# Kernel optimization log

Hardware: AMD Instinct MI355X
Metric: run time of the kernel (lower is better)

Reference implementation:

```python
import jax, jax.numpy as jnp
import numpy as np

C = 32          # in_channels
K = 16          # cluster_nums
G = 16          # grid size per axis (64 / window 4)
FW = 4          # window size
H = G * FW      # 64
NG = G ** 3     # 4096 nodes
NC = NG // K    # 256 nodes per cluster (balanced)
EPS = 1e-5


def setup_inputs():
    key = jax.random.key(0)
    ks = jax.random.split(key, 10)
    def w(k, shape, s=0.05):
        return jax.random.normal(k, shape, jnp.float32) * s
    # balanced cluster assignment (each cluster has exactly NC nodes)
    rng = np.random.RandomState(0)
    ci = np.repeat(np.arange(K, dtype=np.int32), NC)
    rng.shuffle(ci)
    return {
        "x_concat": jax.random.normal(ks[0], (1, H, H, H, C), jnp.float32),
        "cluster_index": jnp.asarray(ci),
        # per-cluster Adjacent_matrix params (1x1 conv == per-pixel linear)
        "conv1_w": w(ks[1], (K, 2 * C, C)), "conv1_b": jnp.zeros((K, 2 * C)),
        "bn1_g": jnp.ones((K, 2 * C)), "bn1_b": jnp.zeros((K, 2 * C)),
        "conv2_w": w(ks[2], (K, 3 * C, 2 * C)), "conv2_b": jnp.zeros((K, 3 * C)),
        "bn2_g": jnp.ones((K, 3 * C)), "bn2_b": jnp.zeros((K, 3 * C)),
        "conv3_w": w(ks[3], (K, 3 * C)), "conv3_b": jnp.zeros((K,)),
        # per-cluster GCN params
        "gcn_w": w(ks[4], (K, 2 * C, C)),
        "bn3_g": jnp.ones((K, C)), "bn3_b": jnp.zeros((K, C)),
        # shared MLP producing spatial weight [C,C] from centroid
        "mlp_w1": w(ks[5], (C, C * C // 8)), "mlp_b1": jnp.zeros((C * C // 8,)),
        "mlp_w2": w(ks[6], (C * C // 8, C * C // 4)), "mlp_b2": jnp.zeros((C * C // 4,)),
        "mlp_w3": w(ks[7], (C * C // 4, C * C)), "mlp_b3": jnp.zeros((C * C,)),
    }


def _bn(h, g, b, axes):
    # train-mode BatchNorm (biased batch statistics), dropout treated as eval/no-op
    m = h.mean(axes, keepdims=True)
    v = h.var(axes, keepdims=True)
    return (h - m) * jax.lax.rsqrt(v + EPS) * g + b


def _forward(cluster_index, x_concat, conv1_w, conv1_b, bn1_g, bn1_b,
             conv2_w, conv2_b, bn2_g, bn2_b, conv3_w, conv3_b,
             gcn_w, bn3_g, bn3_b,
             mlp_w1, mlp_b1, mlp_w2, mlp_b2, mlp_w3, mlp_b3):
    # window_partition + mean over windows -> [NG, C] node features
    x = x_concat.reshape(1, G, FW, G, FW, G, FW, C).mean(axis=(2, 4, 6)).reshape(NG, C)
    order = jnp.argsort(cluster_index)  # stable: contiguous per-cluster index blocks
    eye = jnp.eye(NC, dtype=x.dtype)
    outs = []
    for i in range(K):  # fixed structural loop over clusters
        idx = order[i * NC:(i + 1) * NC]
        xi = x[idx]                                  # [n, C]
        cent = xi.mean(0)                            # kmeans centroid of cluster
        h = jax.nn.relu(cent @ mlp_w1 + mlp_b1)
        h = jax.nn.relu(h @ mlp_w2 + mlp_b2)
        sw = jax.nn.sigmoid(h @ mlp_w3 + mlp_b3).reshape(C, C)
        # Adjacent_matrix: pairwise |xi - xj| -> 1x1 conv stack -> softmax adjacency
        d = jnp.abs(xi[:, None, :] - xi[None, :, :])  # [n, n, C]
        a = jax.nn.leaky_relu(_bn(jnp.einsum('ijc,oc->ijo', d, conv1_w[i]) + conv1_b[i],
                                  bn1_g[i], bn1_b[i], (0, 1)), 0.2)
        a = jax.nn.leaky_relu(_bn(jnp.einsum('ijc,oc->ijo', a, conv2_w[i]) + conv2_b[i],
                                  bn2_g[i], bn2_b[i], (0, 1)), 0.2)
        logits = jnp.einsum('ijc,c->ij', a, conv3_w[i]) + conv3_b[i]  # symmetric
        adj = jax.nn.softmax(logits - 1e8 * eye, axis=-1)
        # gmul_GCN with edge ops [eye, adj] -> concat([x, adj @ x])
        agg = jnp.concatenate([xi, adj @ xi], axis=-1)  # [n, 2C]
        hi = jax.nn.leaky_relu(agg @ (gcn_w[i] @ sw), 0.2)
        hi = _bn(hi, bn3_g[i], bn3_b[i], (0,))          # BatchNorm1d over nodes
        outs.append(hi)
    # scatter_restore
    x_new = jnp.zeros((NG, C), x.dtype).at[order].set(jnp.concatenate(outs, 0))
    # back to grid, pad (1,2) per spatial dim, unfold 4-windows stride 1
    xg = x_new.reshape(1, G, G, G, C).transpose(0, 4, 1, 2, 3)  # [1,C,G,G,G]
    xp = jnp.pad(xg, ((0, 0), (0, 0), (1, 2), (1, 2), (1, 2)))
    iw = jnp.arange(G)[:, None] + jnp.arange(FW)[None, :]       # [G, FW]
    t = xp[:, :, iw]          # [1,C,G,FW,Gp,Gp]
    t = t[:, :, :, :, iw]     # [1,C,G,FW,G,FW,Gp]
    t = t[..., iw]            # [1,C,G,FW,G,FW,G,FW]
    out = t.transpose(0, 2, 3, 4, 5, 6, 7, 1).reshape(1, H, H, H, C)
    return out + x_concat


def reference(x_concat, cluster_index, conv1_w, conv1_b, bn1_g, bn1_b,
              conv2_w, conv2_b, bn2_g, bn2_b, conv3_w, conv3_b,
              gcn_w, bn3_g, bn3_b,
              mlp_w1, mlp_b1, mlp_w2, mlp_b2, mlp_w3, mlp_b3):
    return _forward(cluster_index, x_concat, conv1_w, conv1_b, bn1_g, bn1_b,
                    conv2_w, conv2_b, bn2_g, bn2_b, conv3_w, conv3_b,
                    gcn_w, bn3_g, bn3_b,
                    mlp_w1, mlp_b1, mlp_w2, mlp_b2, mlp_w3, mlp_b3)
```

## Files before the change

### kernel.cpp

```cpp
#include <hip/hip_runtime.h>
#include <hip/hip_bf16.h>


typedef short bfrag8 __attribute__((ext_vector_type(8)));
typedef float f32x4  __attribute__((ext_vector_type(4)));
typedef int   i32x4  __attribute__((ext_vector_type(4)));
typedef short s4v    __attribute__((ext_vector_type(4)));

#define DI __device__ __forceinline__

DI unsigned short f2bf(float f) {
  return __builtin_bit_cast(unsigned short, __float2bfloat16(f));
}
DI float bf2f(unsigned short u) {
  return __builtin_bit_cast(float, ((unsigned)u) << 16);
}
DI unsigned pack2bf(float lo, float hi) {
  unsigned ulo = __builtin_bit_cast(unsigned, lo) + 0x8000u;
  unsigned uhi = __builtin_bit_cast(unsigned, hi) + 0x8000u;
  return __builtin_amdgcn_perm(uhi, ulo, 0x07060302u);
}
DI bfrag8 scale_frag(bfrag8 v, float sc) {
  i32x4 wi = __builtin_bit_cast(i32x4, v);
  i32x4 o;
#pragma unroll
  for (int j = 0; j < 4; ++j) {
    unsigned u = (unsigned)wi[j];
    float lo = bf2f((unsigned short)(u & 0xffffu));
    float hi = bf2f((unsigned short)(u >> 16));
    o[j] = (int)pack2bf(lo * sc, hi * sc);
  }
  return __builtin_bit_cast(bfrag8, o);
}

__global__ __launch_bounds__(256) void k_prep(
    const float* __restrict__ xc, float* __restrict__ x,
    const float* __restrict__ w1, const float* __restrict__ w2,
    unsigned short* __restrict__ w1b, unsigned short* __restrict__ w2p,
    float* __restrict__ statsz) {
  const int bid = blockIdx.x, tid = threadIdx.x;
  if (bid < 128) {
    int idx = bid * 256 + tid;
    int c4 = idx & 7, g = idx >> 3;
    int gz = g & 15, gy = (g >> 4) & 15, gx = g >> 8;
    f32x4 s = {0.f, 0.f, 0.f, 0.f};
    for (int ix = 0; ix < 4; ++ix)
      for (int iy = 0; iy < 4; ++iy)
        for (int iz = 0; iz < 4; ++iz) {
          int X = gx * 4 + ix, Y = gy * 4 + iy, Z = gz * 4 + iz;
          s += *(const f32x4*)&xc[(size_t)(((X << 6) | Y) << 6 | Z) * 32 + c4 * 4];
        }
    *(f32x4*)&x[(size_t)idx * 4] = s * (1.f / 64.f);
    if (bid < 24) statsz[bid * 256 + tid] = 0.f;
  } else {
    int i = (bid - 128) * 256 + tid;
    if (i < 32768) w1b[i] = f2bf(w1[i]);
    int o = i >> 6, cc = i & 63;
    int s = cc >> 5, kp = cc & 31;
    int src = 32 * s + 16 * ((kp >> 2) & 1) + 4 * (kp >> 3) + (kp & 3);
    w2p[i] = f2bf(w2[(size_t)o * 64 + src]);
  }
}

__global__ __launch_bounds__(256) void k_order(
    const int* __restrict__ ci, const float* __restrict__ x,
    int* __restrict__ order, int* __restrict__ inv, float* __restrict__ xi,
    unsigned short* __restrict__ xib, float* __restrict__ centb) {
  const int k = blockIdx.x, t = threadIdx.x;
  __shared__ int scnt[256];
  __shared__ int ordl[256];
  __shared__ unsigned short xls[256 * 36];
  __shared__ float red[256];

  int match[16];
  int cnt = 0;
#pragma unroll
  for (int j = 0; j < 16; ++j) { match[j] = (ci[t * 16 + j] == k); cnt += match[j]; }
  scnt[t] = cnt;
  __syncthreads();
  for (int off = 1; off < 256; off <<= 1) {
    int v = (t >= off) ? scnt[t - off] : 0;
    __syncthreads();
    scnt[t] += v;
    __syncthreads();
  }
  int pos = scnt[t] - cnt;
#pragma unroll
  for (int j = 0; j < 16; ++j)
    if (match[j]) ordl[pos++] = t * 16 + j;
  __syncthreads();
  int src = ordl[t];
  order[k * 256 + t] = src;
  inv[src] = k * 256 + t;
  const f32x4* xr = (const f32x4*)(x + (size_t)src * 32);
  f32x4* xo = (f32x4*)(xi + ((size_t)k * 256 + t) * 32);
  uint2* xb = (uint2*)(xib + ((size_t)k * 256 + t) * 32);
  uint2* xl = (uint2*)&xls[t * 36];
#pragma unroll
  for (int c = 0; c < 8; ++c) {
    f32x4 v = xr[c];
    xo[c] = v;
    unsigned int lo = f2bf(v[0]) | ((unsigned)f2bf(v[1]) << 16);
    unsigned int hi = f2bf(v[2]) | ((unsigned)f2bf(v[3]) << 16);
    xb[c] = make_uint2(lo, hi);
    xl[c] = make_uint2(lo, hi);
  }
  __syncthreads();

  {
    int c = t & 31, rp = t >> 5;
    float ssum = 0.f;
    for (int r = rp; r < 256; r += 8) ssum += bf2f(xls[r * 36 + c]);
    red[t] = ssum;
  }
  __syncthreads();
  if (t < 32) {
    float tot = 0.f;
#pragma unroll
    for (int g = 0; g < 8; ++g) tot += red[g * 32 + t];
    centb[k * 32 + t] = tot * (1.f / 256.f);
  }
}

__global__ __launch_bounds__(256) void k_mlp(
    const float* __restrict__ centb,
    const float* __restrict__ mw1, const float* __restrict__ mb1,
    const float* __restrict__ mw2, const float* __restrict__ mb2,
    const float* __restrict__ mw3, const float* __restrict__ mb3,
    float* __restrict__ swb) {
  const int k = blockIdx.y, bx = blockIdx.x, t = threadIdx.x;
  __shared__ float cent[32];
  __shared__ float h1[128];
  __shared__ float h2s[256];
  __shared__ float red[256];
  if (t < 32) cent[t] = centb[k * 32 + t];
  __syncthreads();
  if (t < 128) {
    float s = mb1[t];
#pragma unroll
    for (int c = 0; c < 32; ++c) s += cent[c] * mw1[c * 128 + t];
    h1[t] = fmaxf(s, 0.f);
  }
  __syncthreads();
  {
    float s = mb2[t];
    for (int j = 0; j < 128; ++j) s += h1[j] * mw2[j * 256 + t];
    h2s[t] = fmaxf(s, 0.f);
  }
  __syncthreads();
  const int o = bx * 64 + (t & 63);
  const int part = t >> 6;
  float s = 0.f;
  const float* m3 = mw3 + (size_t)(part * 64) * 1024 + o;
#pragma unroll 8
  for (int j = 0; j < 64; ++j) s += h2s[part * 64 + j] * m3[j * 1024];
  red[t] = s;
  __syncthreads();
  if (t < 64) {
    float tot = red[t] + red[t + 64] + red[t + 128] + red[t + 192] + mb3[o];
    swb[k * 1024 + o] = 1.f / (1.f + __expf(-tot));
  }
}

template <int MODE>
__global__ __launch_bounds__(256, (MODE == 1) ? 3 : 4) void k_conv01(
    const float* __restrict__ xi,
    const unsigned short* __restrict__ w1b,
    const unsigned short* __restrict__ w2p,
    float* stats1, float* stats2,
    const float* __restrict__ bn1g, const float* __restrict__ bn1b) {
  const int k   = blockIdx.y;
  const int t36 = blockIdx.x;
  int a = 0, rem = t36;
  while (rem >= 8 - a) { rem -= 8 - a; ++a; }
  const int b = a + rem;
  const float w = (a == b) ? 1.f : 2.f;

  const int tid = threadIdx.x;
  const int lane = tid & 63;
  const int wv  = tid >> 6;
  const int l15 = lane & 15;
  const int lg  = lane >> 4;
  const int Pb0 = a * 32, Qb = b * 32;

  constexpr int NF  = (MODE == 0) ? 4 : 6;
  constexpr int NCH = NF * 4;

  __shared__ __align__(16) float xp[32][32];
  __shared__ float sred[192];
  __shared__ __align__(16) float s1s[(MODE == 1) ? 64 : 1];
  __shared__ __align__(16) float t1s[(MODE == 1) ? 64 : 1];

  const float* xik = xi + (size_t)k * 8192;
  {
    int r = tid >> 3, c4 = (tid & 7) * 4;
    *(f32x4*)&xp[r][c4] = *(const f32x4*)(xik + (size_t)(Pb0 + r) * 32 + c4);
  }
  if (tid < 192) sred[tid] = 0.f;
  if constexpr (MODE == 1) {
    if (tid >= 192) {
      const int ch = tid - 192;
      float sum = stats1[k * 128 + 2 * ch], sqv = stats1[k * 128 + 2 * ch + 1];
      float mean = sum * (1.f / 16384.f);
      float var  = sqv * (1.f / 16384.f) - mean * mean;
      float s = bn1g[k * 64 + ch] * rsqrtf(fmaxf(var, 0.f) + 1e-5f);
      s1s[ch] = s;
      t1s[ch] = bn1b[k * 64 + ch] - mean * s;
    }
  }

  float qv[2][8];
#pragma unroll
  for (int qg = 0; qg < 2; ++qg) {
    const f32x4* src = (const f32x4*)(xik + (size_t)(Qb + qg * 16 + l15) * 32 + lg * 8);
    f32x4 v0 = src[0], v1 = src[1];
#pragma unroll
    for (int j = 0; j < 4; ++j) { qv[qg][j] = v0[j]; qv[qg][4 + j] = v1[j]; }
  }

  bfrag8 B1[4];
  {
    const unsigned short* w1k = w1b + k * 2048;
#pragma unroll
    for (int f = 0; f < 4; ++f)
      B1[f] = *(const bfrag8*)(w1k + (16 * f + l15) * 32 + lg * 8);
  }
  bfrag8 B2[6][2];
  if constexpr (MODE == 1) {
    const unsigned short* w2k = w2p + k * 6144;
#pragma unroll
    for (int f2 = 0; f2 < 6; ++f2) {
      B2[f2][0] = *(const bfrag8*)(w2k + (16 * f2 + l15) * 64 + lg * 8);
      B2[f2][1] = *(const bfrag8*)(w2k + (16 * f2 + l15) * 64 + 32 + lg * 8);
    }
  }

  float ss[24], sq[24];
#pragma unroll
  for (int i = 0; i < 24; ++i) { ss[i] = 0.f; sq[i] = 0.f; }

  __syncthreads();

  if constexpr (MODE == 1) {
#pragma unroll
    for (int f = 0; f < 4; ++f)
      B1[f] = scale_frag(B1[f], s1s[16 * f + l15]);
  }

  const f32x4 z = {0.f, 0.f, 0.f, 0.f};

  bfrag8 dfa[4];
#pragma unroll
  for (int rp = 0; rp < 4; ++rp) {
    const int pl = rp >> 1, qg = rp & 1;
    const int plocal = wv * 8 + pl * 4;
    const float* xpp = &xp[plocal][lg * 8];
    f32x4 p0 = *(const f32x4*)xpp;
    f32x4 p1 = *(const f32x4*)(xpp + 4);
    float pvv[8];
#pragma unroll
    for (int j = 0; j < 4; ++j) { pvv[j] = p0[j]; pvv[4 + j] = p1[j]; }
    unsigned dw[4];
#pragma unroll
    for (int wj = 0; wj < 4; ++wj) {
      float d0 = fabsf(qv[qg][2 * wj]     - pvv[2 * wj]);
      float d1 = fabsf(qv[qg][2 * wj + 1] - pvv[2 * wj + 1]);
      dw[wj] = pack2bf(d0, d1);
    }
    i32x4 dwi = {(int)dw[0], (int)dw[1], (int)dw[2], (int)dw[3]};
    dfa[rp] = __builtin_bit_cast(bfrag8, dwi);
  }

#pragma unroll
  for (int rp = 0; rp < 4; ++rp) {
    f32x4 acc1[4];
    __builtin_amdgcn_s_setprio(1);
#pragma unroll
    for (int f = 0; f < 4; ++f) {
      f32x4 cin;
      if constexpr (MODE == 0) cin = z;
      else cin = *(const f32x4*)&t1s[16 * f + 4 * lg];
      acc1[f] = __builtin_amdgcn_mfma_f32_16x16x32_bf16(B1[f], dfa[rp], cin, 0, 0, 0);
    }
    __builtin_amdgcn_s_setprio(0);

    if constexpr (MODE == 0) {
#pragma unroll
      for (int f = 0; f < 4; ++f)
#pragma unroll
        for (int r = 0; r < 4; ++r) {
          float h = acc1[f][r];
          ss[f * 4 + r] += h; sq[f * 4 + r] = fmaf(h, h, sq[f * 4 + r]);
        }
    } else {
      unsigned paw[8];
#pragma unroll
      for (int f = 0; f < 4; ++f) {
        float h0 = acc1[f][0], h1 = acc1[f][1], h2 = acc1[f][2], h3 = acc1[f][3];
        h0 = fmaxf(h0, 0.2f * h0); h1 = fmaxf(h1, 0.2f * h1);
        h2 = fmaxf(h2, 0.2f * h2); h3 = fmaxf(h3, 0.2f * h3);
        paw[f * 2]     = pack2bf(h0, h1);
        paw[f * 2 + 1] = pack2bf(h2, h3);
      }
      i32x4 pa0i = {(int)paw[0], (int)paw[1], (int)paw[2], (int)paw[3]};
      i32x4 pa1i = {(int)paw[4], (int)paw[5], (int)paw[6], (int)paw[7]};
      bfrag8 pa0 = __builtin_bit_cast(bfrag8, pa0i);
      bfrag8 pa1 = __builtin_bit_cast(bfrag8, pa1i);

      __builtin_amdgcn_s_setprio(1);
#pragma unroll
      for (int f2 = 0; f2 < 6; ++f2) {
        f32x4 acc = __builtin_amdgcn_mfma_f32_16x16x32_bf16(B2[f2][0], pa0, z, 0, 0, 0);
        acc = __builtin_amdgcn_mfma_f32_16x16x32_bf16(B2[f2][1], pa1, acc, 0, 0, 0);
#pragma unroll
        for (int r = 0; r < 4; ++r) {
          float h = acc[r];
          ss[f2 * 4 + r] += h; sq[f2 * 4 + r] = fmaf(h, h, sq[f2 * 4 + r]);
        }
      }
      __builtin_amdgcn_s_setprio(0);
    }
  }

#pragma unroll
  for (int i = 0; i < NCH; ++i) {
#pragma unroll
    for (int m = 1; m <= 8; m <<= 1) {
      ss[i] += __shfl_xor(ss[i], m);
      sq[i] += __shfl_xor(sq[i], m);
    }
  }
  if (l15 == 0) {
#pragma unroll
    for (int i = 0; i < NCH; ++i) {
      int ch = 16 * (i >> 2) + 4 * lg + (i & 3);
      atomicAdd(&sred[ch * 2 + 0], ss[i] * w);
      atomicAdd(&sred[ch * 2 + 1], sq[i] * w);
    }
  }
  __syncthreads();
  float* gs = (MODE == 0) ? stats1 : stats2;
  if (tid < 2 * 16 * NF) atomicAdd(&gs[k * (2 * 16 * NF) + tid], sred[tid]);
}

__global__ __launch_bounds__(256, 4) void k_conv2(
    const float* __restrict__ xi,
    const unsigned short* __restrict__ w1b,
    const unsigned short* __restrict__ w2p,
    const float* __restrict__ stats1, const float* __restrict__ stats2,
    const float* __restrict__ bn1g, const float* __restrict__ bn1b,
    const float* __restrict__ bn2g, const float* __restrict__ bn2b,
    const float* __restrict__ c3w,
    float* __restrict__ logits) {
  const int k  = blockIdx.y;
  const int bx = blockIdx.x;
  const int tid = threadIdx.x;
  const int lane = tid & 63;
  const int wv  = tid >> 6;
  const int l15 = lane & 15;
  const int lg  = lane >> 4;

  __shared__ __align__(16) float xp[16][32];
  __shared__ __align__(16) float s1s[64];
  __shared__ __align__(16) float t1s[64];
  __shared__ __align__(16) float sw2s[96];
  __shared__ __align__(16) float cb2s[96];
  __shared__ __align__(16) float s42s[96];
  __shared__ float lt[16][17];

  const float* xik = xi + (size_t)k * 8192;

  if (tid < 64) {
    const int ch = tid;
    float sum = stats1[k * 128 + 2 * ch], sqv = stats1[k * 128 + 2 * ch + 1];
    float mean = sum * (1.f / 16384.f);
    float var  = sqv * (1.f / 16384.f) - mean * mean;
    float s = bn1g[k * 64 + ch] * rsqrtf(fmaxf(var, 0.f) + 1e-5f);
    s1s[ch] = s;
    t1s[ch] = bn1b[k * 64 + ch] - mean * s;
  } else if (tid < 160) {
    const int ch = tid - 64;
    float sum = stats2[k * 192 + 2 * ch], sqv = stats2[k * 192 + 2 * ch + 1];
    float mean = sum * (1.f / 16384.f);
    float var  = sqv * (1.f / 16384.f) - mean * mean;
    float s2 = bn2g[k * 96 + ch] * rsqrtf(fmaxf(var, 0.f) + 1e-5f);
    float t2 = bn2b[k * 96 + ch] - mean * s2;
    float w3 = c3w[k * 96 + ch];
    sw2s[ch] = s2 * w3;
    cb2s[ch] = t2 * w3;
    s42s[ch] = copysignf(0.4f, w3);
  }

  bfrag8 B1[4];
  {
    const unsigned short* w1k = w1b + k * 2048;
#pragma unroll
    for (int f = 0; f < 4; ++f)
      B1[f] = *(const bfrag8*)(w1k + (16 * f + l15) * 32 + lg * 8);
  }
  bfrag8 B2[6][2];
  {
    const unsigned short* w2k = w2p + k * 6144;
#pragma unroll
    for (int f2 = 0; f2 < 6; ++f2) {
      B2[f2][0] = *(const bfrag8*)(w2k + (16 * f2 + l15) * 64 + lg * 8);
      B2[f2][1] = *(const bfrag8*)(w2k + (16 * f2 + l15) * 64 + 32 + lg * 8);
    }
  }
  __syncthreads();
#pragma unroll
  for (int f = 0; f < 4; ++f)
    B1[f] = scale_frag(B1[f], s1s[16 * f + l15]);
#pragma unroll
  for (int f2 = 0; f2 < 6; ++f2) {
    float sc = sw2s[16 * f2 + l15];
    B2[f2][0] = scale_frag(B2[f2][0], sc);
    B2[f2][1] = scale_frag(B2[f2][1], sc);
  }

  for (int st = bx; st < 144; st += 64) {
    const int t36 = st >> 2, sub = st & 3;
    int a = 0, rem = t36;
    while (rem >= 8 - a) { rem -= 8 - a; ++a; }
    const int b = a + rem;
    const int Pb0 = a * 32 + (sub >> 1) * 16;
    const int Qb  = b * 32 + (sub & 1) * 16;

    __syncthreads();
    if (tid < 128) {
      int r = tid >> 3, c4 = (tid & 7) * 4;
      *(f32x4*)&xp[r][c4] = *(const f32x4*)(xik + (size_t)(Pb0 + r) * 32 + c4);
    }
    __syncthreads();

    float qv8[8];
    {
      const f32x4* src = (const f32x4*)(xik + (size_t)(Qb + l15) * 32 + lg * 8);
      f32x4 v0 = src[0], v1 = src[1];
#pragma unroll
      for (int j = 0; j < 4; ++j) { qv8[j] = v0[j]; qv8[4 + j] = v1[j]; }
    }

#pragma unroll
    for (int rp = 0; rp < 4; ++rp) {
      const int plocal = wv * 4 + rp;
      const int pglob  = Pb0 + plocal;

      const float* xpp = &xp[plocal][lg * 8];
      f32x4 p0 = *(const f32x4*)xpp;
      f32x4 p1 = *(const f32x4*)(xpp + 4);
      float pvv[8];
#pragma unroll
      for (int j = 0; j < 4; ++j) { pvv[j] = p0[j]; pvv[4 + j] = p1[j]; }
      unsigned dw[4];
#pragma unroll
      for (int wj = 0; wj < 4; ++wj) {
        float d0 = fabsf(qv8[2 * wj]     - pvv[2 * wj]);
        float d1 = fabsf(qv8[2 * wj + 1] - pvv[2 * wj + 1]);
        dw[wj] = pack2bf(d0, d1);
      }
      i32x4 dwi = {(int)dw[0], (int)dw[1], (int)dw[2], (int)dw[3]};
      bfrag8 df = __builtin_bit_cast(bfrag8, dwi);

      f32x4 acc1[4];
      __builtin_amdgcn_s_setprio(1);
#pragma unroll
      for (int f = 0; f < 4; ++f) {
        f32x4 cin = *(const f32x4*)&t1s[16 * f + 4 * lg];
        acc1[f] = __builtin_amdgcn_mfma_f32_16x16x32_bf16(B1[f], df, cin, 0, 0, 0);
      }
      __builtin_amdgcn_s_setprio(0);

      unsigned paw[8];
#pragma unroll
      for (int f = 0; f < 4; ++f) {
        float h0 = acc1[f][0], h1 = acc1[f][1], h2 = acc1[f][2], h3 = acc1[f][3];
        h0 = fmaxf(h0, 0.2f * h0); h1 = fmaxf(h1, 0.2f * h1);
        h2 = fmaxf(h2, 0.2f * h2); h3 = fmaxf(h3, 0.2f * h3);
        paw[f * 2]     = pack2bf(h0, h1);
        paw[f * 2 + 1] = pack2bf(h2, h3);
      }
      i32x4 pa0i = {(int)paw[0], (int)paw[1], (int)paw[2], (int)paw[3]};
      i32x4 pa1i = {(int)paw[4], (int)paw[5], (int)paw[6], (int)paw[7]};
      bfrag8 pa0 = __builtin_bit_cast(bfrag8, pa0i);
      bfrag8 pa1 = __builtin_bit_cast(bfrag8, pa1i);

      float lp = 0.f;
      __builtin_amdgcn_s_setprio(1);
#pragma unroll
      for (int f2 = 0; f2 < 6; ++f2) {
        f32x4 cin = *(const f32x4*)&cb2s[16 * f2 + 4 * lg];
        f32x4 acc = __builtin_amdgcn_mfma_f32_16x16x32_bf16(B2[f2][0], pa0, cin, 0, 0, 0);
        acc = __builtin_amdgcn_mfma_f32_16x16x32_bf16(B2[f2][1], pa1, acc, 0, 0, 0);
        f32x4 s4 = *(const f32x4*)&s42s[16 * f2 + 4 * lg];
#pragma unroll
        for (int r = 0; r < 4; ++r) {
          float aa = acc[r];
          float ab = fmaxf(aa, -aa);
          lp = fmaf(0.6f, aa, lp);
          lp = fmaf(s4[r], ab, lp);
        }
      }
      __builtin_amdgcn_s_setprio(0);
      lp += __shfl_xor(lp, 16);
      lp += __shfl_xor(lp, 32);
      if (lg == 0) {
        logits[(size_t)k * 65536 + (size_t)pglob * 256 + Qb + l15] = lp;
        lt[plocal][l15] = lp;
      }
    }

    __syncthreads();
    if (a != b) {
      const int ql = tid >> 4, pl = tid & 15;
      logits[(size_t)k * 65536 + (size_t)(Qb + ql) * 256 + Pb0 + pl] = lt[pl][ql];
    }
  }
}

__global__ __launch_bounds__(256) void k_graph(
    const unsigned short* __restrict__ xib,
    const float* __restrict__ logits,
    const float* __restrict__ swb,
    const float* __restrict__ gcnw,
    float* __restrict__ hi,
    float* __restrict__ stats3) {
  const int k  = blockIdx.y;
  const int pc = blockIdx.x;
  const int tid = threadIdx.x;
  __shared__ __align__(16) unsigned char smem[40960];
  unsigned short* xis = (unsigned short*)smem;
  float* wks  = (float*)(smem + 20480);
  float* cbuf = (float*)(smem + 28672);

  {
    const s4v* src = (const s4v*)(xib + (size_t)k * 8192 + tid * 32);
    s4v* dst = (s4v*)&xis[tid * 40];
#pragma unroll
    for (int j = 0; j < 8; ++j) dst[j] = src[j];
  }
  float* swl = cbuf;
  float* gks = cbuf + 1024;
#pragma unroll
  for (int j = 0; j < 4; ++j) swl[tid + j * 256] = swb[k * 1024 + tid + j * 256];
#pragma unroll
  for (int j = 0; j < 8; ++j) gks[tid + j * 256] = gcnw[(size_t)k * 2048 + tid + j * 256];
  __syncthreads();

#pragma unroll
  for (int j = 0; j < 8; ++j) {
    int e = tid + j * 256;
    int u = e >> 5, v = e & 31;
    float s = 0.f;
#pragma unroll
    for (int c = 0; c < 32; ++c) s += gks[u * 32 + c] * swl[c * 32 + v];
    wks[e] = s;
  }
  __syncthreads();

  float* es    = cbuf;
  float* axs   = cbuf + 2080;
  float* inv_s = cbuf + 2352;
  float* s3    = cbuf + 2360;
  if (tid < 64) s3[tid] = 0.f;

  const int row = tid >> 5;
  const int s   = tid & 31;
  const int pglob = pc * 8 + row;
  const float* lrow = logits + (size_t)k * 65536 + (size_t)pglob * 256;

  float m = -1e30f;
  for (int q = s; q < 256; q += 32) {
    float v = lrow[q];
    m = (q == pglob) ? m : fmaxf(m, v);
  }
#pragma unroll
  for (int mm = 1; mm < 32; mm <<= 1) m = fmaxf(m, __shfl_xor(m, mm));
  float sum = 0.f;
  for (int q = s; q < 256; q += 32) {
    float e = (q == pglob) ? 0.f : __expf(lrow[q] - m);
    es[row * 260 + q] = e;
    sum += e;
  }
#pragma unroll
  for (int mm = 1; mm < 32; mm <<= 1) sum += __shfl_xor(sum, mm);
  if (s == 0) inv_s[row] = 1.f / sum;
  __syncthreads();

  float a0 = 0.f;
  for (int q = 0; q < 256; ++q)
    a0 += es[row * 260 + q] * bf2f(xis[q * 40 + s]);
  axs[row * 34 + s] = a0 * inv_s[row];
  __syncthreads();

  float h = 0.f;
  for (int u = 0; u < 32; ++u) {
    float xu = bf2f(xis[pglob * 40 + u]);
    float au = axs[row * 34 + u];
    h += xu * wks[u * 32 + s] + au * wks[(32 + u) * 32 + s];
  }
  float v = fmaxf(h, 0.2f * h);
  hi[(size_t)k * 8192 + (size_t)pglob * 32 + s] = v;
  float vs = v, vq = v * v;
  vs += __shfl_xor(vs, 32);
  vq += __shfl_xor(vq, 32);
  if ((tid & 32) == 0) {
    atomicAdd(&s3[s * 2 + 0], vs);
    atomicAdd(&s3[s * 2 + 1], vq);
  }
  __syncthreads();
  if (tid < 64) atomicAdd(&stats3[k * 64 + tid], s3[tid]);
}

__global__ __launch_bounds__(256) void k_final(
    const float* __restrict__ xc, const float* __restrict__ hi,
    const float* __restrict__ stats3,
    const float* __restrict__ g3, const float* __restrict__ b3,
    const int* __restrict__ inv, float* __restrict__ out) {
  const int tid = threadIdx.x;
  __shared__ float cs[512], ct[512];
#pragma unroll
  for (int j = 0; j < 2; ++j) {
    int ch = tid * 2 + j;
    int kk = ch >> 5, c = ch & 31;
    float sum = stats3[kk * 64 + c * 2], sqv = stats3[kk * 64 + c * 2 + 1];
    float mean = sum * (1.f / 256.f);
    float var = sqv * (1.f / 256.f) - mean * mean;
    float s = g3[kk * 32 + c] * rsqrtf(fmaxf(var, 0.f) + 1e-5f);
    cs[ch] = s;
    ct[ch] = b3[kk * 32 + c] - mean * s;
  }
  __syncthreads();

  int idx = blockIdx.x * 256 + tid;
  int c4 = idx & 7, v = idx >> 3;
  int z = v & 63, y = (v >> 6) & 63, x = v >> 12;
  int sx = (x >> 2) + (x & 3) - 1;
  int sy = (y >> 2) + (y & 3) - 1;
  int sz = (z >> 2) + (z & 3) - 1;
  f32x4 add = {0.f, 0.f, 0.f, 0.f};
  if ((unsigned)sx < 16u && (unsigned)sy < 16u && (unsigned)sz < 16u) {
    int fg = ((sx << 4) + sy) * 16 + sz;
    int pi = inv[fg];
    int kk = pi >> 8;
    f32x4 h = *(const f32x4*)&hi[(size_t)pi * 32 + c4 * 4];
    int cb = kk * 32 + c4 * 4;
#pragma unroll
    for (int j = 0; j < 4; ++j) add[j] = h[j] * cs[cb + j] + ct[cb + j];
  }
  const f32x4 a = *(const f32x4*)&xc[(size_t)idx * 4];
  *(f32x4*)&out[(size_t)idx * 4] = a + add;
}

extern "C" void kernel_launch(void* const* d_in, const int* in_sizes, int n_in,
                              void* d_out, int out_size, void* d_ws, size_t ws_size,
                              hipStream_t stream) {
  const float* xc   = (const float*)d_in[0];
  const int*   ci   = (const int*)  d_in[1];
  const float* c1w  = (const float*)d_in[2];
  const float* bn1g = (const float*)d_in[4];
  const float* bn1b = (const float*)d_in[5];
  const float* c2w  = (const float*)d_in[6];
  const float* bn2g = (const float*)d_in[8];
  const float* bn2b = (const float*)d_in[9];
  const float* c3w  = (const float*)d_in[10];
  const float* gcnw = (const float*)d_in[12];
  const float* bn3g = (const float*)d_in[13];
  const float* bn3b = (const float*)d_in[14];
  const float* mw1  = (const float*)d_in[15];
  const float* mb1  = (const float*)d_in[16];
  const float* mw2  = (const float*)d_in[17];
  const float* mb2  = (const float*)d_in[18];
  const float* mw3  = (const float*)d_in[19];
  const float* mb3  = (const float*)d_in[20];

  float* wsf = (float*)d_ws;
  float*  x      = wsf + 0;
  float*  xi     = wsf + 131072;
  float*  hi     = wsf + 393216;
  float*  swb    = wsf + 524288;
  float*  stats1 = wsf + 557056;
  float*  stats2 = wsf + 559104;
  float*  stats3 = wsf + 562176;
  float*  centb  = wsf + 563200;
  float*  logits = wsf + 567296;
  unsigned char* wsb = (unsigned char*)d_ws;
  int* order = (int*)(wsb + 6463488);
  unsigned short* w1b = (unsigned short*)(wsb + 6463488 + 16384);
  unsigned short* w2p = (unsigned short*)(wsb + 6463488 + 16384 + 65536);
  unsigned short* xib = (unsigned short*)(wsb + 6463488 + 16384 + 65536 + 196608);
  int* inv = (int*)(wsb + 6463488 + 16384 + 65536 + 196608 + 262144);

  k_prep <<<512, 256, 0, stream>>>(xc, x, c1w, c2w, w1b, w2p, stats1);
  k_order<<<16, 256, 0, stream>>>(ci, x, order, inv, xi, xib, centb);
  k_mlp  <<<dim3(16, 16), 256, 0, stream>>>(centb, mw1, mb1, mw2, mb2, mw3, mb3, swb);
  k_conv01<0><<<dim3(36, 16), 256, 0, stream>>>(xi, w1b, w2p, stats1, stats2, bn1g, bn1b);
  k_conv01<1><<<dim3(36, 16), 256, 0, stream>>>(xi, w1b, w2p, stats1, stats2, bn1g, bn1b);
  k_conv2<<<dim3(64, 16), 256, 0, stream>>>(xi, w1b, w2p, stats1, stats2,
                                            bn1g, bn1b, bn2g, bn2b, c3w, logits);
  k_graph<<<dim3(32, 16), 256, 0, stream>>>(xib, logits, swb, gcnw, hi, stats3);
  k_final<<<8192, 256, 0, stream>>>(xc, hi, stats3, bn3g, bn3b, inv, (float*)d_out);
}
```

Before: 104.9 us.

## Fuse MLP into conv0 launch and flatten conv2 grid to one tile per block

Result: faster. 97.50 us (-7.1%).

```diff
diff --git a/kernel.cpp b/kernel.cpp
--- a/kernel.cpp
+++ b/kernel.cpp
@@ -122,52 +122,162 @@
   }
 }
 
-__global__ __launch_bounds__(256) void k_mlp(
+__global__ __launch_bounds__(256, 4) void k_c0mlp(
+    const float* __restrict__ xi,
+    const unsigned short* __restrict__ w1b,
+    float* stats1,
     const float* __restrict__ centb,
     const float* __restrict__ mw1, const float* __restrict__ mb1,
     const float* __restrict__ mw2, const float* __restrict__ mb2,
     const float* __restrict__ mw3, const float* __restrict__ mb3,
     float* __restrict__ swb) {
-  const int k = blockIdx.y, bx = blockIdx.x, t = threadIdx.x;
+  const int k = blockIdx.y;
+  const int tid = threadIdx.x;
+  __shared__ __align__(16) float xp[32][32];
+  __shared__ float sred[256];
   __shared__ float cent[32];
   __shared__ float h1[128];
   __shared__ float h2s[256];
-  __shared__ float red[256];
-  if (t < 32) cent[t] = centb[k * 32 + t];
-  __syncthreads();
-  if (t < 128) {
-    float s = mb1[t];
-#pragma unroll
-    for (int c = 0; c < 32; ++c) s += cent[c] * mw1[c * 128 + t];
-    h1[t] = fmaxf(s, 0.f);
-  }
-  __syncthreads();
-  {
-    float s = mb2[t];
-    for (int j = 0; j < 128; ++j) s += h1[j] * mw2[j * 256 + t];
-    h2s[t] = fmaxf(s, 0.f);
-  }
-  __syncthreads();
-  const int o = bx * 64 + (t & 63);
-  const int part = t >> 6;
-  float s = 0.f;
-  const float* m3 = mw3 + (size_t)(part * 64) * 1024 + o;
+
+  if (blockIdx.x >= 36) {
+    const int bx = blockIdx.x - 36;
+    if (tid < 32) cent[tid] = centb[k * 32 + tid];
+    __syncthreads();
+    if (tid < 128) {
+      float s = mb1[tid];
+#pragma unroll
+      for (int c = 0; c < 32; ++c) s += cent[c] * mw1[c * 128 + tid];
+      h1[tid] = fmaxf(s, 0.f);
+    }
+    __syncthreads();
+    {
+      float s = mb2[tid];
+      for (int j = 0; j < 128; ++j) s += h1[j] * mw2[j * 256 + tid];
+      h2s[tid] = fmaxf(s, 0.f);
+    }
+    __syncthreads();
+    const int o = bx * 64 + (tid & 63);
+    const int part = tid >> 6;
+    float s = 0.f;
+    const float* m3 = mw3 + (size_t)(part * 64) * 1024 + o;
 #pragma unroll 8
-  for (int j = 0; j < 64; ++j) s += h2s[part * 64 + j] * m3[j * 1024];
-  red[t] = s;
-  __syncthreads();
-  if (t < 64) {
-    float tot = red[t] + red[t + 64] + red[t + 128] + red[t + 192] + mb3[o];
-    swb[k * 1024 + o] = 1.f / (1.f + __expf(-tot));
-  }
-}
-
-template <int MODE>
-__global__ __launch_bounds__(256, (MODE == 1) ? 3 : 4) void k_conv01(
+    for (int j = 0; j < 64; ++j) s += h2s[part * 64 + j] * m3[j * 1024];
+    sred[tid] = s;
+    __syncthreads();
+    if (tid < 64) {
+      float tot = sred[tid] + sred[tid + 64] + sred[tid + 128] + sred[tid + 192] + mb3[o];
+      swb[k * 1024 + o] = 1.f / (1.f + __expf(-tot));
+    }
+    return;
+  }
+
+  const int t36 = blockIdx.x;
+  int a = 0, rem = t36;
+  while (rem >= 8 - a) { rem -= 8 - a; ++a; }
+  const int b = a + rem;
+  const float w = (a == b) ? 1.f : 2.f;
+
+  const int lane = tid & 63;
+  const int wv  = tid >> 6;
+  const int l15 = lane & 15;
+  const int lg  = lane >> 4;
+  const int Pb0 = a * 32, Qb = b * 32;
+
+  const float* xik = xi + (size_t)k * 8192;
+  {
+    int r = tid >> 3, c4 = (tid & 7) * 4;
+    *(f32x4*)&xp[r][c4] = *(const f32x4*)(xik + (size_t)(Pb0 + r) * 32 + c4);
+  }
+  if (tid < 128) sred[tid] = 0.f;
+
+  float qv[2][8];
+#pragma unroll
+  for (int qg = 0; qg < 2; ++qg) {
+    const f32x4* src = (const f32x4*)(xik + (size_t)(Qb + qg * 16 + l15) * 32 + lg * 8);
+    f32x4 v0 = src[0], v1 = src[1];
+#pragma unroll
+    for (int j = 0; j < 4; ++j) { qv[qg][j] = v0[j]; qv[qg][4 + j] = v1[j]; }
+  }
+
+  bfrag8 B1[4];
+  {
+    const unsigned short* w1k = w1b + k * 2048;
+#pragma unroll
+    for (int f = 0; f < 4; ++f)
+      B1[f] = *(const bfrag8*)(w1k + (16 * f + l15) * 32 + lg * 8);
+  }
+
+  float ss[16], sq[16];
+#pragma unroll
+  for (int i = 0; i < 16; ++i) { ss[i] = 0.f; sq[i] = 0.f; }
+
+  __syncthreads();
+
+  const f32x4 z = {0.f, 0.f, 0.f, 0.f};
+  bfrag8 dfa[4];
+#pragma unroll
+  for (int rp = 0; rp < 4; ++rp) {
+    const int pl = rp >> 1, qg = rp & 1;
+    const int plocal = wv * 8 + pl * 4;
+    const float* xpp = &xp[plocal][lg * 8];
+    f32x4 p0 = *(const f32x4*)xpp;
+    f32x4 p1 = *(const f32x4*)(xpp + 4);
+    float pvv[8];
+#pragma unroll
+    for (int j = 0; j < 4; ++j) { pvv[j] = p0[j]; pvv[4 + j] = p1[j]; }
+    unsigned dw[4];
+#pragma unroll
+    for (int wj = 0; wj < 4; ++wj) {
+      float d0 = fabsf(qv[qg][2 * wj]     - pvv[2 * wj]);
+      float d1 = fabsf(qv[qg][2 * wj + 1] - pvv[2 * wj + 1]);
+      dw[wj] = pack2bf(d0, d1);
+    }
+    i32x4 dwi = {(int)dw[0], (int)dw[1], (int)dw[2], (int)dw[3]};
+    dfa[rp] = __builtin_bit_cast(bfrag8, dwi);
+  }
+
+#pragma unroll
+  for (int rp = 0; rp < 4; ++rp) {
+    f32x4 acc1[4];
+    __builtin_amdgcn_s_setprio(1);
+#pragma unroll
+    for (int f = 0; f < 4; ++f)
+      acc1[f] = __builtin_amdgcn_mfma_f32_16x16x32_bf16(B1[f], dfa[rp], z, 0, 0, 0);
+    __builtin_amdgcn_s_setprio(0);
+#pragma unroll
+    for (int f = 0; f < 4; ++f)
+#pragma unroll
+      for (int r = 0; r < 4; ++r) {
+        float h = acc1[f][r];
+        ss[f * 4 + r] += h; sq[f * 4 + r] = fmaf(h, h, sq[f * 4 + r]);
+      }
+  }
+
+#pragma unroll
+  for (int i = 0; i < 16; ++i) {
+#pragma unroll
+    for (int m = 1; m <= 8; m <<= 1) {
+      ss[i] += __shfl_xor(ss[i], m);
+      sq[i] += __shfl_xor(sq[i], m);
+    }
+  }
+  if (l15 == 0) {
+#pragma unroll
+    for (int i = 0; i < 16; ++i) {
+      int ch = 16 * (i >> 2) + 4 * lg + (i & 3);
+      atomicAdd(&sred[ch * 2 + 0], ss[i] * w);
+      atomicAdd(&sred[ch * 2 + 1], sq[i] * w);
+    }
+  }
+  __syncthreads();
+  if (tid < 128) atomicAdd(&stats1[k * 128 + tid], sred[tid]);
+}
+
+__global__ __launch_bounds__(256, 3) void k_conv1(
     const float* __restrict__ xi,
     const unsigned short* __restrict__ w1b,
     const unsigned short* __restrict__ w2p,
-    float* stats1, float* stats2,
+    const float* __restrict__ stats1, float* stats2,
     const float* __restrict__ bn1g, const float* __restrict__ bn1b) {
   const int k   = blockIdx.y;
   const int t36 = blockIdx.x;
@@ -183,13 +293,10 @@
   const int lg  = lane >> 4;
   const int Pb0 = a * 32, Qb = b * 32;
 
-  constexpr int NF  = (MODE == 0) ? 4 : 6;
-  constexpr int NCH = NF * 4;
-
   __shared__ __align__(16) float xp[32][32];
   __shared__ float sred[192];
-  __shared__ __align__(16) float s1s[(MODE == 1) ? 64 : 1];
-  __shared__ __align__(16) float t1s[(MODE == 1) ? 64 : 1];
+  __shared__ __align__(16) float s1s[64];
+  __shared__ __align__(16) float t1s[64];
 
   const float* xik = xi + (size_t)k * 8192;
   {
@@ -197,16 +304,14 @@
     *(f32x4*)&xp[r][c4] = *(const f32x4*)(xik + (size_t)(Pb0 + r) * 32 + c4);
   }
   if (tid < 192) sred[tid] = 0.f;
-  if constexpr (MODE == 1) {
-    if (tid >= 192) {
-      const int ch = tid - 192;
-      float sum = stats1[k * 128 + 2 * ch], sqv = stats1[k * 128 + 2 * ch + 1];
-      float mean = sum * (1.f / 16384.f);
-      float var  = sqv * (1.f / 16384.f) - mean * mean;
-      float s = bn1g[k * 64 + ch] * rsqrtf(fmaxf(var, 0.f) + 1e-5f);
-      s1s[ch] = s;
-      t1s[ch] = bn1b[k * 64 + ch] - mean * s;
-    }
+  if (tid >= 192) {
+    const int ch = tid - 192;
+    float sum = stats1[k * 128 + 2 * ch], sqv = stats1[k * 128 + 2 * ch + 1];
+    float mean = sum * (1.f / 16384.f);
+    float var  = sqv * (1.f / 16384.f) - mean * mean;
+    float s = bn1g[k * 64 + ch] * rsqrtf(fmaxf(var, 0.f) + 1e-5f);
+    s1s[ch] = s;
+    t1s[ch] = bn1b[k * 64 + ch] - mean * s;
   }
 
   float qv[2][8];
@@ -226,7 +331,7 @@
       B1[f] = *(const bfrag8*)(w1k + (16 * f + l15) * 32 + lg * 8);
   }
   bfrag8 B2[6][2];
-  if constexpr (MODE == 1) {
+  {
     const unsigned short* w2k = w2p + k * 6144;
 #pragma unroll
     for (int f2 = 0; f2 < 6; ++f2) {
@@ -241,11 +346,9 @@
 
   __syncthreads();
 
-  if constexpr (MODE == 1) {
-#pragma unroll
-    for (int f = 0; f < 4; ++f)
-      B1[f] = scale_frag(B1[f], s1s[16 * f + l15]);
-  }
+#pragma unroll
+  for (int f = 0; f < 4; ++f)
+    B1[f] = scale_frag(B1[f], s1s[16 * f + l15]);
 
   const f32x4 z = {0.f, 0.f, 0.f, 0.f};
 
@@ -277,53 +380,41 @@
     __builtin_amdgcn_s_setprio(1);
 #pragma unroll
     for (int f = 0; f < 4; ++f) {
-      f32x4 cin;
-      if constexpr (MODE == 0) cin = z;
-      else cin = *(const f32x4*)&t1s[16 * f + 4 * lg];
+      f32x4 cin = *(const f32x4*)&t1s[16 * f + 4 * lg];
       acc1[f] = __builtin_amdgcn_mfma_f32_16x16x32_bf16(B1[f], dfa[rp], cin, 0, 0, 0);
     }
     __builtin_amdgcn_s_setprio(0);
 
-    if constexpr (MODE == 0) {
-#pragma unroll
-      for (int f = 0; f < 4; ++f)
-#pragma unroll
-        for (int r = 0; r < 4; ++r) {
-          float h = acc1[f][r];
-          ss[f * 4 + r] += h; sq[f * 4 + r] = fmaf(h, h, sq[f * 4 + r]);
-        }
-    } else {
-      unsigned paw[8];
-#pragma unroll
-      for (int f = 0; f < 4; ++f) {
-        float h0 = acc1[f][0], h1 = acc1[f][1], h2 = acc1[f][2], h3 = acc1[f][3];
-        h0 = fmaxf(h0, 0.2f * h0); h1 = fmaxf(h1, 0.2f * h1);
-        h2 = fmaxf(h2, 0.2f * h2); h3 = fmaxf(h3, 0.2f * h3);
-        paw[f * 2]     = pack2bf(h0, h1);
-        paw[f * 2 + 1] = pack2bf(h2, h3);
+    unsigned paw[8];
+#pragma unroll
+    for (int f = 0; f < 4; ++f) {
+      float h0 = acc1[f][0], h1 = acc1[f][1], h2 = acc1[f][2], h3 = acc1[f][3];
+      h0 = fmaxf(h0, 0.2f * h0); h1 = fmaxf(h1, 0.2f * h1);
+      h2 = fmaxf(h2, 0.2f * h2); h3 = fmaxf(h3, 0.2f * h3);
+      paw[f * 2]     = pack2bf(h0, h1);
+      paw[f * 2 + 1] = pack2bf(h2, h3);
+    }
+    i32x4 pa0i = {(int)paw[0], (int)paw[1], (int)paw[2], (int)paw[3]};
+    i32x4 pa1i = {(int)paw[4], (int)paw[5], (int)paw[6], (int)paw[7]};
+    bfrag8 pa0 = __builtin_bit_cast(bfrag8, pa0i);
+    bfrag8 pa1 = __builtin_bit_cast(bfrag8, pa1i);
+
+    __builtin_amdgcn_s_setprio(1);
+#pragma unroll
+    for (int f2 = 0; f2 < 6; ++f2) {
+      f32x4 acc = __builtin_amdgcn_mfma_f32_16x16x32_bf16(B2[f2][0], pa0, z, 0, 0, 0);
+      acc = __builtin_amdgcn_mfma_f32_16x16x32_bf16(B2[f2][1], pa1, acc, 0, 0, 0);
+#pragma unroll
+      for (int r = 0; r < 4; ++r) {
+        float h = acc[r];
+        ss[f2 * 4 + r] += h; sq[f2 * 4 + r] = fmaf(h, h, sq[f2 * 4 + r]);
       }
-      i32x4 pa0i = {(int)paw[0], (int)paw[1], (int)paw[2], (int)paw[3]};
-      i32x4 pa1i = {(int)paw[4], (int)paw[5], (int)paw[6], (int)paw[7]};
-      bfrag8 pa0 = __builtin_bit_cast(bfrag8, pa0i);
-      bfrag8 pa1 = __builtin_bit_cast(bfrag8, pa1i);
-
-      __builtin_amdgcn_s_setprio(1);
-#pragma unroll
-      for (int f2 = 0; f2 < 6; ++f2) {
-        f32x4 acc = __builtin_amdgcn_mfma_f32_16x16x32_bf16(B2[f2][0], pa0, z, 0, 0, 0);
-        acc = __builtin_amdgcn_mfma_f32_16x16x32_bf16(B2[f2][1], pa1, acc, 0, 0, 0);
-#pragma unroll
-        for (int r = 0; r < 4; ++r) {
-          float h = acc[r];
-          ss[f2 * 4 + r] += h; sq[f2 * 4 + r] = fmaf(h, h, sq[f2 * 4 + r]);
-        }
-      }
-      __builtin_amdgcn_s_setprio(0);
-    }
-  }
-
-#pragma unroll
-  for (int i = 0; i < NCH; ++i) {
+    }
+    __builtin_amdgcn_s_setprio(0);
+  }
+
+#pragma unroll
+  for (int i = 0; i < 24; ++i) {
 #pragma unroll
     for (int m = 1; m <= 8; m <<= 1) {
       ss[i] += __shfl_xor(ss[i], m);
@@ -332,15 +423,14 @@
   }
   if (l15 == 0) {
 #pragma unroll
-    for (int i = 0; i < NCH; ++i) {
+    for (int i = 0; i < 24; ++i) {
       int ch = 16 * (i >> 2) + 4 * lg + (i & 3);
       atomicAdd(&sred[ch * 2 + 0], ss[i] * w);
       atomicAdd(&sred[ch * 2 + 1], sq[i] * w);
     }
   }
   __syncthreads();
-  float* gs = (MODE == 0) ? stats1 : stats2;
-  if (tid < 2 * 16 * NF) atomicAdd(&gs[k * (2 * 16 * NF) + tid], sred[tid]);
+  if (tid < 192) atomicAdd(&stats2[k * 192 + tid], sred[tid]);
 }
 
 __global__ __launch_bounds__(256, 4) void k_conv2(
@@ -352,8 +442,15 @@
     const float* __restrict__ bn2g, const float* __restrict__ bn2b,
     const float* __restrict__ c3w,
     float* __restrict__ logits) {
-  const int k  = blockIdx.y;
-  const int bx = blockIdx.x;
+  const int k   = blockIdx.y;
+  const int t36 = blockIdx.x >> 2;
+  const int sub = blockIdx.x & 3;
+  int a = 0, rem = t36;
+  while (rem >= 8 - a) { rem -= 8 - a; ++a; }
+  const int b = a + rem;
+  const int Pb0 = a * 32 + (sub >> 1) * 16;
+  const int Qb  = b * 32 + (sub & 1) * 16;
+
   const int tid = threadIdx.x;
   const int lane = tid & 63;
   const int wv  = tid >> 6;
@@ -370,25 +467,39 @@
 
   const float* xik = xi + (size_t)k * 8192;
 
-  if (tid < 64) {
-    const int ch = tid;
+  if (tid < 128) {
+    int r = tid >> 3, c4 = (tid & 7) * 4;
+    *(f32x4*)&xp[r][c4] = *(const f32x4*)(xik + (size_t)(Pb0 + r) * 32 + c4);
+  } else if (tid < 192) {
+    const int ch = tid - 128;
     float sum = stats1[k * 128 + 2 * ch], sqv = stats1[k * 128 + 2 * ch + 1];
     float mean = sum * (1.f / 16384.f);
     float var  = sqv * (1.f / 16384.f) - mean * mean;
     float s = bn1g[k * 64 + ch] * rsqrtf(fmaxf(var, 0.f) + 1e-5f);
     s1s[ch] = s;
     t1s[ch] = bn1b[k * 64 + ch] - mean * s;
-  } else if (tid < 160) {
-    const int ch = tid - 64;
-    float sum = stats2[k * 192 + 2 * ch], sqv = stats2[k * 192 + 2 * ch + 1];
-    float mean = sum * (1.f / 16384.f);
-    float var  = sqv * (1.f / 16384.f) - mean * mean;
-    float s2 = bn2g[k * 96 + ch] * rsqrtf(fmaxf(var, 0.f) + 1e-5f);
-    float t2 = bn2b[k * 96 + ch] - mean * s2;
-    float w3 = c3w[k * 96 + ch];
-    sw2s[ch] = s2 * w3;
-    cb2s[ch] = t2 * w3;
-    s42s[ch] = copysignf(0.4f, w3);
+  }
+  {
+    int ch = tid - 160;
+    if (ch >= 0 && ch < 96) {
+      float sum = stats2[k * 192 + 2 * ch], sqv = stats2[k * 192 + 2 * ch + 1];
+      float mean = sum * (1.f / 16384.f);
+      float var  = sqv * (1.f / 16384.f) - mean * mean;
+      float s2 = bn2g[k * 96 + ch] * rsqrtf(fmaxf(var, 0.f) + 1e-5f);
+      float t2 = bn2b[k * 96 + ch] - mean * s2;
+      float w3 = c3w[k * 96 + ch];
+      sw2s[ch] = s2 * w3;
+      cb2s[ch] = t2 * w3;
+      s42s[ch] = copysignf(0.4f, w3);
+    }
+  }
+
+  float qv8[8];
+  {
+    const f32x4* src = (const f32x4*)(xik + (size_t)(Qb + l15) * 32 + lg * 8);
+    f32x4 v0 = src[0], v1 = src[1];
+#pragma unroll
+    for (int j = 0; j < 4; ++j) { qv8[j] = v0[j]; qv8[4 + j] = v1[j]; }
   }
 
   bfrag8 B1[4];
@@ -418,103 +529,79 @@
     B2[f2][1] = scale_frag(B2[f2][1], sc);
   }
 
-  for (int st = bx; st < 144; st += 64) {
-    const int t36 = st >> 2, sub = st & 3;
-    int a = 0, rem = t36;
-    while (rem >= 8 - a) { rem -= 8 - a; ++a; }
-    const int b = a + rem;
-    const int Pb0 = a * 32 + (sub >> 1) * 16;
-    const int Qb  = b * 32 + (sub & 1) * 16;
-
+#pragma unroll
+  for (int rp = 0; rp < 4; ++rp) {
+    const int plocal = wv * 4 + rp;
+    const int pglob  = Pb0 + plocal;
+
+    const float* xpp = &xp[plocal][lg * 8];
+    f32x4 p0 = *(const f32x4*)xpp;
+    f32x4 p1 = *(const f32x4*)(xpp + 4);
+    float pvv[8];
+#pragma unroll
+    for (int j = 0; j < 4; ++j) { pvv[j] = p0[j]; pvv[4 + j] = p1[j]; }
+    unsigned dw[4];
+#pragma unroll
+    for (int wj = 0; wj < 4; ++wj) {
+      float d0 = fabsf(qv8[2 * wj]     - pvv[2 * wj]);
+      float d1 = fabsf(qv8[2 * wj + 1] - pvv[2 * wj + 1]);
+      dw[wj] = pack2bf(d0, d1);
+    }
+    i32x4 dwi = {(int)dw[0], (int)dw[1], (int)dw[2], (int)dw[3]};
+    bfrag8 df = __builtin_bit_cast(bfrag8, dwi);
+
+    f32x4 acc1[4];
+    __builtin_amdgcn_s_setprio(1);
+#pragma unroll
+    for (int f = 0; f < 4; ++f) {
+      f32x4 cin = *(const f32x4*)&t1s[16 * f + 4 * lg];
+      acc1[f] = __builtin_amdgcn_mfma_f32_16x16x32_bf16(B1[f], df, cin, 0, 0, 0);
+    }
+    __builtin_amdgcn_s_setprio(0);
+
+    unsigned paw[8];
+#pragma unroll
+    for (int f = 0; f < 4; ++f) {
+      float h0 = acc1[f][0], h1 = acc1[f][1], h2 = acc1[f][2], h3 = acc1[f][3];
+      h0 = fmaxf(h0, 0.2f * h0); h1 = fmaxf(h1, 0.2f * h1);
+      h2 = fmaxf(h2, 0.2f * h2); h3 = fmaxf(h3, 0.2f * h3);
+      paw[f * 2]     = pack2bf(h0, h1);
+      paw[f * 2 + 1] = pack2bf(h2, h3);
+    }
+    i32x4 pa0i = {(int)paw[0], (int)paw[1], (int)paw[2], (int)paw[3]};
+    i32x4 pa1i = {(int)paw[4], (int)paw[5], (int)paw[6], (int)paw[7]};
+    bfrag8 pa0 = __builtin_bit_cast(bfrag8, pa0i);
+    bfrag8 pa1 = __builtin_bit_cast(bfrag8, pa1i);
+
+    float lp = 0.f;
+    __builtin_amdgcn_s_setprio(1);
+#pragma unroll
+    for (int f2 = 0; f2 < 6; ++f2) {
+      f32x4 cin = *(const f32x4*)&cb2s[16 * f2 + 4 * lg];
+      f32x4 acc = __builtin_amdgcn_mfma_f32_16x16x32_bf16(B2[f2][0], pa0, cin, 0, 0, 0);
+      acc = __builtin_amdgcn_mfma_f32_16x16x32_bf16(B2[f2][1], pa1, acc, 0, 0, 0);
+      f32x4 s4 = *(const f32x4*)&s42s[16 * f2 + 4 * lg];
+#pragma unroll
+      for (int r = 0; r < 4; ++r) {
+        float aa = acc[r];
+        float ab = fmaxf(aa, -aa);
+        lp = fmaf(0.6f, aa, lp);
+        lp = fmaf(s4[r], ab, lp);
+      }
+    }
+    __builtin_amdgcn_s_setprio(0);
+    lp += __shfl_xor(lp, 16);
+    lp += __shfl_xor(lp, 32);
+    if (lg == 0) {
+      logits[(size_t)k * 65536 + (size_t)pglob * 256 + Qb + l15] = lp;
+      lt[plocal][l15] = lp;
+    }
+  }
+
+  if (a != b) {
     __syncthreads();
-    if (tid < 128) {
-      int r = tid >> 3, c4 = (tid & 7) * 4;
-      *(f32x4*)&xp[r][c4] = *(const f32x4*)(xik + (size_t)(Pb0 + r) * 32 + c4);
-    }
-    __syncthreads();
-
-    float qv8[8];
-    {
-      const f32x4* src = (const f32x4*)(xik + (size_t)(Qb + l15) * 32 + lg * 8);
-      f32x4 v0 = src[0], v1 = src[1];
-#pragma unroll
-      for (int j = 0; j < 4; ++j) { qv8[j] = v0[j]; qv8[4 + j] = v1[j]; }
-    }
-
-#pragma unroll
-    for (int rp = 0; rp < 4; ++rp) {
-      const int plocal = wv * 4 + rp;
-      const int pglob  = Pb0 + plocal;
-
-      const float* xpp = &xp[plocal][lg * 8];
-      f32x4 p0 = *(const f32x4*)xpp;
-      f32x4 p1 = *(const f32x4*)(xpp + 4);
-      float pvv[8];
-#pragma unroll
-      for (int j = 0; j < 4; ++j) { pvv[j] = p0[j]; pvv[4 + j] = p1[j]; }
-      unsigned dw[4];
-#pragma unroll
-      for (int wj = 0; wj < 4; ++wj) {
-        float d0 = fabsf(qv8[2 * wj]     - pvv[2 * wj]);
-        float d1 = fabsf(qv8[2 * wj + 1] - pvv[2 * wj + 1]);
-        dw[wj] = pack2bf(d0, d1);
-      }
-      i32x4 dwi = {(int)dw[0], (int)dw[1], (int)dw[2], (int)dw[3]};
-      bfrag8 df = __builtin_bit_cast(bfrag8, dwi);
-
-      f32x4 acc1[4];
-      __builtin_amdgcn_s_setprio(1);
-#pragma unroll
-      for (int f = 0; f < 4; ++f) {
-        f32x4 cin = *(const f32x4*)&t1s[16 * f + 4 * lg];
-        acc1[f] = __builtin_amdgcn_mfma_f32_16x16x32_bf16(B1[f], df, cin, 0, 0, 0);
-      }
-      __builtin_amdgcn_s_setprio(0);
-
-      unsigned paw[8];
-#pragma unroll
-      for (int f = 0; f < 4; ++f) {
-        float h0 = acc1[f][0], h1 = acc1[f][1], h2 = acc1[f][2], h3 = acc1[f][3];
-        h0 = fmaxf(h0, 0.2f * h0); h1 = fmaxf(h1, 0.2f * h1);
-        h2 = fmaxf(h2, 0.2f * h2); h3 = fmaxf(h3, 0.2f * h3);
-        paw[f * 2]     = pack2bf(h0, h1);
-        paw[f * 2 + 1] = pack2bf(h2, h3);
-      }
-      i32x4 pa0i = {(int)paw[0], (int)paw[1], (int)paw[2], (int)paw[3]};
-      i32x4 pa1i = {(int)paw[4], (int)paw[5], (int)paw[6], (int)paw[7]};
-      bfrag8 pa0 = __builtin_bit_cast(bfrag8, pa0i);
-      bfrag8 pa1 = __builtin_bit_cast(bfrag8, pa1i);
-
-      float lp = 0.f;
-      __builtin_amdgcn_s_setprio(1);
-#pragma unroll
-      for (int f2 = 0; f2 < 6; ++f2) {
-        f32x4 cin = *(const f32x4*)&cb2s[16 * f2 + 4 * lg];
-        f32x4 acc = __builtin_amdgcn_mfma_f32_16x16x32_bf16(B2[f2][0], pa0, cin, 0, 0, 0);
-        acc = __builtin_amdgcn_mfma_f32_16x16x32_bf16(B2[f2][1], pa1, acc, 0, 0, 0);
-        f32x4 s4 = *(const f32x4*)&s42s[16 * f2 + 4 * lg];
-#pragma unroll
-        for (int r = 0; r < 4; ++r) {
-          float aa = acc[r];
-          float ab = fmaxf(aa, -aa);
-          lp = fmaf(0.6f, aa, lp);
-          lp = fmaf(s4[r], ab, lp);
-        }
-      }
-      __builtin_amdgcn_s_setprio(0);
-      lp += __shfl_xor(lp, 16);
-      lp += __shfl_xor(lp, 32);
-      if (lg == 0) {
-        logits[(size_t)k * 65536 + (size_t)pglob * 256 + Qb + l15] = lp;
-        lt[plocal][l15] = lp;
-      }
-    }
-
-    __syncthreads();
-    if (a != b) {
-      const int ql = tid >> 4, pl = tid & 15;
-      logits[(size_t)k * 65536 + (size_t)(Qb + ql) * 256 + Pb0 + pl] = lt[pl][ql];
-    }
+    const int ql = tid >> 4, pl = tid & 15;
+    logits[(size_t)k * 65536 + (size_t)(Qb + ql) * 256 + Pb0 + pl] = lt[pl][ql];
   }
 }
 
@@ -693,11 +780,11 @@
 
   k_prep <<<512, 256, 0, stream>>>(xc, x, c1w, c2w, w1b, w2p, stats1);
   k_order<<<16, 256, 0, stream>>>(ci, x, order, inv, xi, xib, centb);
-  k_mlp  <<<dim3(16, 16), 256, 0, stream>>>(centb, mw1, mb1, mw2, mb2, mw3, mb3, swb);
-  k_conv01<0><<<dim3(36, 16), 256, 0, stream>>>(xi, w1b, w2p, stats1, stats2, bn1g, bn1b);
-  k_conv01<1><<<dim3(36, 16), 256, 0, stream>>>(xi, w1b, w2p, stats1, stats2, bn1g, bn1b);
-  k_conv2<<<dim3(64, 16), 256, 0, stream>>>(xi, w1b, w2p, stats1, stats2,
-                                            bn1g, bn1b, bn2g, bn2b, c3w, logits);
+  k_c0mlp<<<dim3(52, 16), 256, 0, stream>>>(xi, w1b, stats1, centb,
+                                            mw1, mb1, mw2, mb2, mw3, mb3, swb);
+  k_conv1<<<dim3(36, 16), 256, 0, stream>>>(xi, w1b, w2p, stats1, stats2, bn1g, bn1b);
+  k_conv2<<<dim3(144, 16), 256, 0, stream>>>(xi, w1b, w2p, stats1, stats2,
+                                             bn1g, bn1b, bn2g, bn2b, c3w, logits);
   k_graph<<<dim3(32, 16), 256, 0, stream>>>(xib, logits, swb, gcnw, hi, stats3);
   k_final<<<8192, 256, 0, stream>>>(xc, hi, stats3, bn3g, bn3b, inv, (float*)d_out);
 }
```
